# Optimization experiments

Hardware: AMD Instinct MI355X
Metric: run time of the kernel (lower is better)

## Reference

```python
import jax, jax.numpy as jnp
import numpy as np

B, N, M, K, H = 32, 2048, 16, 32, 2
EPS = 1e-7


def setup_inputs() -> dict:
    key = jax.random.key(0)
    k1, k2, k3, k4, k5 = jax.random.split(key, 5)
    coords = jax.random.normal(k1, (B, N, M), jnp.float32)
    hom = jax.random.randint(k2, (B, N), 0, H).astype(jnp.float32)
    # ragged lengths: valid points first, all-zero padding rows after
    lengths = jax.random.randint(k3, (B,), N // 2, N + 1)
    rowmask = (jnp.arange(N)[None, :] < lengths[:, None]).astype(jnp.float32)
    dgm = jnp.concatenate([hom[..., None], coords], axis=-1) * rowmask[..., None]
    # tf.random_normal_initializer default stddev = 0.05
    theta = 0.05 * jax.random.normal(k4, (K, M), jnp.float32)
    class_w = 0.05 * jax.random.normal(k5, (H,), jnp.float32)
    return {"dgm": dgm, "theta": theta, "class_w": class_w}


def reference(dgm, theta, class_w):
    # dgm: [B, N, M+1]; dgm[:,:,0] = homology class, rest = point coords
    b, n = dgm.shape[0], dgm.shape[1]
    k, m = theta.shape
    hom = jnp.clip(dgm[:, :, 0].astype(jnp.int32), 0, class_w.shape[0] - 1)  # [B,N]
    y = dgm[:, :, 1:]                                                        # [B,N,m]
    # while-loop semantics: process points until the FIRST all-zero row
    nonzero = jnp.any(dgm != 0, axis=-1)
    valid = jnp.cumprod(nonzero.astype(dgm.dtype), axis=1)                   # [B,N]
    w = class_w[hom] * valid                                                 # [B,N]
    # Poincare parametrization: z = theta_k * y, map R^m -> ball via z/(1+sqrt(1+|z|^2))
    z = y[:, None, :, :] * theta[None, :, None, :]                           # [B,K,N,m]
    zn2 = jnp.sum(z * z, axis=-1, keepdims=True)
    x = z / (1.0 + jnp.sqrt(1.0 + zn2))                                      # in unit ball
    # log map at origin (c=1): artanh(|x|) * x / |x|
    xn = jnp.sqrt(jnp.sum(x * x, axis=-1, keepdims=True))
    v = jnp.arctanh(jnp.minimum(xn, 1.0 - EPS)) * x / jnp.maximum(xn, EPS)   # [B,K,N,m]
    # per-(diagram, basis) class-weighted tangent sum
    T = jnp.einsum('bknm,bn->bkm', v, w)                                     # [B,K,m]
    # FAITHFUL to source: `sum` is never reset -> cumulative over (i, k) ordering
    S = jnp.cumsum(T.reshape(b * k, m), axis=0).reshape(b, k, m)
    # exp map at origin (c=1): tanh(|S|) * S / |S|
    sn = jnp.sqrt(jnp.sum(S * S, axis=-1, keepdims=True))
    xd = jnp.tanh(sn) * S / jnp.maximum(sn, EPS)
    yd = 2.0 * xd / (1.0 - jnp.sum(xd * xd, axis=-1, keepdims=True))
    return yd.reshape(b, k * m)
```

## Files before the change

### kernel.cpp

```cpp
#include <hip/hip_runtime.h>
#include <hip/hip_bf16.h>

constexpr int Bc = 32;
constexpr int Nc = 2048;
constexpr int Mc = 16;
constexpr int Kc = 32;
constexpr int ROWc = 17;
constexpr int CH = 256;
constexpr int NCH = Nc / CH;
constexpr int KQ = 8;
constexpr int NKQ = Kc / KQ;
constexpr float EPSc = 1e-7f;
constexpr float HALF_LN2 = 0.34657359028f;

__global__ __launch_bounds__(256) void k_T(const float* __restrict__ dgm,
                                           const float* __restrict__ theta,
                                           const float* __restrict__ class_w,
                                           float* __restrict__ P,
                                           int H) {
    __shared__ float stage[CH * 20];
    __shared__ float red[4 * KQ * 17];

    int bid = blockIdx.x;
    int b   = bid >> 5;
    int rem = bid & 31;
    int kq  = rem >> 3;
    int c   = rem & 7;
    int tid = threadIdx.x;
    int k8  = tid & 7;
    int rg  = tid >> 3;

    const float4* src4 = (const float4*)(dgm + ((size_t)b * Nc + c * CH) * ROWc);
    for (int i = tid; i < (CH * ROWc) / 4; i += 256) {
        float4 v = src4[i];
        unsigned g = 4u * i;
#pragma unroll
        for (int e = 0; e < 4; ++e) {
            unsigned ge  = g + e;
            unsigned row = ge / 17u;
            unsigned col = ge - row * 17u;
            float val = (e == 0) ? v.x : (e == 1) ? v.y : (e == 2) ? v.z : v.w;
            stage[row * 20 + (col == 0 ? 0u : col + 3u)] = val;
        }
    }

    int kg = kq * KQ + k8;
    float th2[16];
    {
        const float4* t4 = (const float4*)theta;
#pragma unroll
        for (int q = 0; q < 4; ++q) {
            float4 tv = t4[kg * 4 + q];
            th2[4*q+0] = tv.x * tv.x; th2[4*q+1] = tv.y * tv.y;
            th2[4*q+2] = tv.z * tv.z; th2[4*q+3] = tv.w * tv.w;
        }
    }
    float cw0 = class_w[0];
    float cw1 = (H > 1) ? class_w[1] : cw0;

    __syncthreads();

    float acc[16];
#pragma unroll
    for (int m = 0; m < 16; ++m) acc[m] = 0.0f;

#pragma unroll
    for (int j = 0; j < 8; ++j) {
        int row = rg * 8 + j;
        const float* rp = &stage[row * 20];
        float r0 = rp[0];
        float r[16];
        {
            float4* rv = (float4*)r;
            const float4* lp = (const float4*)(rp + 4);
            rv[0] = lp[0]; rv[1] = lp[1]; rv[2] = lp[2]; rv[3] = lp[3];
        }

        int h = (int)r0;
        h = max(0, min(h, H - 1));
        float wv = (H == 2) ? (h ? cw1 : cw0) : class_w[h];

        float za = 0.f, zb = 0.f, zc = 0.f, zd = 0.f;
#pragma unroll
        for (int m = 0; m < 16; m += 4) {
            za = fmaf(r[m]   * r[m],   th2[m],   za);
            zb = fmaf(r[m+1] * r[m+1], th2[m+1], zb);
            zc = fmaf(r[m+2] * r[m+2], th2[m+2], zc);
            zd = fmaf(r[m+3] * r[m+3], th2[m+3], zd);
        }
        float zn2 = (za + zb) + (zc + zd);
        float rs  = rsqrtf(fmaxf(zn2, 1e-30f));
        float zn  = zn2 * rs;
        float s   = sqrtf(1.0f + zn2);
        float at2 = __log2f(zn + s);
        float coef = HALF_LN2 * at2 * rs * wv;
#pragma unroll
        for (int m = 0; m < 16; ++m) acc[m] = fmaf(coef, r[m], acc[m]);
    }

#pragma unroll
    for (int m = 0; m < 16; ++m) {
        acc[m] += __shfl_xor(acc[m], 8);
        acc[m] += __shfl_xor(acc[m], 16);
        acc[m] += __shfl_xor(acc[m], 32);
    }

    int w = tid >> 6;
    if ((tid & 63) < 8) {
#pragma unroll
        for (int m = 0; m < 16; ++m) red[w * (KQ * 17) + k8 * 17 + m] = acc[m];
    }
    __syncthreads();

    if (tid < KQ * 16) {
        int kk = tid >> 4;
        int mm = tid & 15;
        float s = 0.0f;
#pragma unroll
        for (int w2 = 0; w2 < 4; ++w2) s += red[w2 * (KQ * 17) + kk * 17 + mm];
        float val = s * theta[kq * 128 + tid];
        P[((size_t)b * 4096 + (size_t)kq * 1024 + (size_t)kk * 128 + mm * 8) + c] = val;
    }
}

__global__ __launch_bounds__(1024) void k_scan(const float* __restrict__ P,
                                               float* __restrict__ out) {
    __shared__ float buf[2][64][Mc];

    int tid = threadIdx.x;
    int m   = tid & 15;
    int seg = tid >> 4;

    float p[16];
    float run = 0.0f;
#pragma unroll
    for (int j = 0; j < 16; ++j) {
        int row = seg * 16 + j;
        const float4* q = (const float4*)(P + (size_t)row * 128 + m * 8);
        float4 a = q[0];
        float4 bq = q[1];
        run += ((a.x + a.y) + (a.z + a.w)) + ((bq.x + bq.y) + (bq.z + bq.w));
        p[j] = run;
    }

    buf[0][seg][m] = run;
    __syncthreads();
    int src = 0;
#pragma unroll
    for (int d = 1; d < 64; d <<= 1) {
        float v = buf[src][seg][m];
        if (seg >= d) v += buf[src][seg - d][m];
        buf[src ^ 1][seg][m] = v;
        __syncthreads();
        src ^= 1;
    }
    float off = (seg > 0) ? buf[src][seg - 1][m] : 0.0f;

#pragma unroll
    for (int j = 0; j < 16; ++j) {
        float S = off + p[j];
        float sn2 = S * S;
        sn2 += __shfl_xor(sn2, 1);
        sn2 += __shfl_xor(sn2, 2);
        sn2 += __shfl_xor(sn2, 4);
        sn2 += __shfl_xor(sn2, 8);
        float sn = sqrtf(sn2);
        float e  = __expf(2.0f * sn);
        float t  = 1.0f - 2.0f / (e + 1.0f);
        float cc = t / fmaxf(sn, EPSc);
        float sx2 = cc * cc * sn2;
        float yd = 2.0f * cc * S / (1.0f - sx2);
        out[(size_t)(seg * 16 + j) * Mc + m] = yd;
    }
}

extern "C" void kernel_launch(void* const* d_in, const int* in_sizes, int n_in,
                              void* d_out, int out_size, void* d_ws, size_t ws_size,
                              hipStream_t stream) {
    const float* dgm     = (const float*)d_in[0];
    const float* theta   = (const float*)d_in[1];
    const float* class_w = (const float*)d_in[2];
    int H = in_sizes[2];

    float* P   = (float*)d_ws;
    float* out = (float*)d_out;

    k_T<<<Bc * NKQ * NCH, 256, 0, stream>>>(dgm, theta, class_w, P, H);
    k_scan<<<1, 1024, 0, stream>>>(P, out);
}
```

Before: 30.01 us.

## Fuse scan into main kernel with per-block completion flags

Merges the two launches into one kernel. Each block publishes its partial results and sets a release flag, and block 0 spins until all 1024 flags are set before running the cumulative scan and writing the output. It then resets the flags for the next call. This removes the second launch and its gap, but it depends on every block becoming resident while block 0 spins, and the scan now runs on 256 threads with a serial offset loop instead of 1024 threads.

Result: slower. 56.57 us (+88.5%).

```diff
diff --git a/kernel.cpp b/kernel.cpp
--- a/kernel.cpp
+++ b/kernel.cpp
@@ -10,14 +10,18 @@
 constexpr int NCH = Nc / CH;
 constexpr int KQ = 8;
 constexpr int NKQ = Kc / KQ;
+constexpr int NBLK = Bc * NKQ * NCH;
+constexpr unsigned MAGIC = 0x5EEDC0DEu;
 constexpr float EPSc = 1e-7f;
 constexpr float HALF_LN2 = 0.34657359028f;
 
-__global__ __launch_bounds__(256) void k_T(const float* __restrict__ dgm,
-                                           const float* __restrict__ theta,
-                                           const float* __restrict__ class_w,
-                                           float* __restrict__ P,
-                                           int H) {
+__global__ __launch_bounds__(256) void k_all(const float* __restrict__ dgm,
+                                             const float* __restrict__ theta,
+                                             const float* __restrict__ class_w,
+                                             float* __restrict__ P,
+                                             unsigned* __restrict__ flags,
+                                             float* __restrict__ out,
+                                             int H) {
     __shared__ float stage[CH * 20];
     __shared__ float red[4 * KQ * 17];
 
@@ -119,46 +123,53 @@
 #pragma unroll
         for (int w2 = 0; w2 < 4; ++w2) s += red[w2 * (KQ * 17) + kk * 17 + mm];
         float val = s * theta[kq * 128 + tid];
-        P[((size_t)b * 4096 + (size_t)kq * 1024 + (size_t)kk * 128 + mm * 8) + c] = val;
-    }
-}
-
-__global__ __launch_bounds__(1024) void k_scan(const float* __restrict__ P,
-                                               float* __restrict__ out) {
-    __shared__ float buf[2][64][Mc];
-
-    int tid = threadIdx.x;
+        size_t idx = (size_t)b * 4096 + (size_t)kq * 1024 + (size_t)kk * 128 + mm * 8 + c;
+        __hip_atomic_store(&P[idx], val, __ATOMIC_RELAXED, __HIP_MEMORY_SCOPE_AGENT);
+    }
+    __syncthreads();
+    if (tid == 0) {
+        __hip_atomic_store(&flags[bid], MAGIC, __ATOMIC_RELEASE, __HIP_MEMORY_SCOPE_AGENT);
+    }
+
+    if (bid != 0) return;
+
+    {
+        int f0 = tid * 4;
+        for (;;) {
+            bool ok = true;
+#pragma unroll
+            for (int j = 0; j < 4; ++j)
+                ok = ok && (__hip_atomic_load(&flags[f0 + j], __ATOMIC_RELAXED,
+                                              __HIP_MEMORY_SCOPE_AGENT) == MAGIC);
+            if (ok) break;
+            __builtin_amdgcn_s_sleep(1);
+        }
+        __builtin_amdgcn_fence(__ATOMIC_ACQUIRE, "agent");
+    }
+    __syncthreads();
+
     int m   = tid & 15;
     int seg = tid >> 4;
-
-    float p[16];
-    float run = 0.0f;
-#pragma unroll
-    for (int j = 0; j < 16; ++j) {
-        int row = seg * 16 + j;
+    int r0  = seg * 64;
+
+    float tot = 0.0f;
+    for (int j = 0; j < 64; ++j) {
+        const float4* q = (const float4*)(P + (size_t)(r0 + j) * 128 + m * 8);
+        float4 a = q[0], bq = q[1];
+        tot += ((a.x + a.y) + (a.z + a.w)) + ((bq.x + bq.y) + (bq.z + bq.w));
+    }
+    red[seg * 16 + m] = tot;
+    __syncthreads();
+    float off = 0.0f;
+    for (int s2 = 0; s2 < seg; ++s2) off += red[s2 * 16 + m];
+
+    float run = off;
+    for (int j = 0; j < 64; ++j) {
+        int row = r0 + j;
         const float4* q = (const float4*)(P + (size_t)row * 128 + m * 8);
-        float4 a = q[0];
-        float4 bq = q[1];
+        float4 a = q[0], bq = q[1];
         run += ((a.x + a.y) + (a.z + a.w)) + ((bq.x + bq.y) + (bq.z + bq.w));
-        p[j] = run;
-    }
-
-    buf[0][seg][m] = run;
-    __syncthreads();
-    int src = 0;
-#pragma unroll
-    for (int d = 1; d < 64; d <<= 1) {
-        float v = buf[src][seg][m];
-        if (seg >= d) v += buf[src][seg - d][m];
-        buf[src ^ 1][seg][m] = v;
-        __syncthreads();
-        src ^= 1;
-    }
-    float off = (seg > 0) ? buf[src][seg - 1][m] : 0.0f;
-
-#pragma unroll
-    for (int j = 0; j < 16; ++j) {
-        float S = off + p[j];
+        float S = run;
         float sn2 = S * S;
         sn2 += __shfl_xor(sn2, 1);
         sn2 += __shfl_xor(sn2, 2);
@@ -170,8 +181,14 @@
         float cc = t / fmaxf(sn, EPSc);
         float sx2 = cc * cc * sn2;
         float yd = 2.0f * cc * S / (1.0f - sx2);
-        out[(size_t)(seg * 16 + j) * Mc + m] = yd;
-    }
+        out[(size_t)row * Mc + m] = yd;
+    }
+
+    __syncthreads();
+#pragma unroll
+    for (int j = 0; j < 4; ++j)
+        __hip_atomic_store(&flags[tid * 4 + j], 0u, __ATOMIC_RELAXED,
+                           __HIP_MEMORY_SCOPE_AGENT);
 }
 
 extern "C" void kernel_launch(void* const* d_in, const int* in_sizes, int n_in,
@@ -182,9 +199,9 @@
     const float* class_w = (const float*)d_in[2];
     int H = in_sizes[2];
 
-    float* P   = (float*)d_ws;
-    float* out = (float*)d_out;
-
-    k_T<<<Bc * NKQ * NCH, 256, 0, stream>>>(dgm, theta, class_w, P, H);
-    k_scan<<<1, 1024, 0, stream>>>(P, out);
+    float*    P     = (float*)d_ws;
+    unsigned* flags = (unsigned*)((char*)d_ws + (size_t)NBLK * 128 * sizeof(float));
+    float*    out   = (float*)d_out;
+
+    k_all<<<NBLK, 256, 0, stream>>>(dgm, theta, class_w, P, flags, out, H);
 }
```
